# Performance work log

Measured on AMD Instinct MI355X. Metric: run time of the kernel, lower is better.

Reference implementation:

```python
import jax, jax.numpy as jnp
import numpy as np

B, N_MELS, T = 8, 96, 1024
FLUX = 1
N_DIMS = N_MELS * (1 + FLUX)          # 192
C = 32                                 # num_channels
D_MODEL = C * (N_DIMS // 4)            # 1536
N_LAYERS = 4
D_STATE = 16
D_CONV = 4
D_INNER = 2 * D_MODEL                  # 3072 (expand=2)
DT_RANK = -(-D_MODEL // 16)            # 96
N_CLASSES = 5


def setup_inputs() -> dict:
    key = jax.random.key(0)
    ks = iter(jax.random.split(key, 64))
    def rn(shape, scale=0.02):
        return jax.random.normal(next(ks), shape, dtype=jnp.float32) * scale
    p = {}
    p['x'] = jax.random.normal(next(ks), (B, N_MELS, T), dtype=jnp.float32)
    # ResidualBlock 1: conv3x3 -> act -> conv3x3, 1x1 shortcut (channel change 1->C)
    p['c1a_w'] = rn((C, 1, 3, 3)); p['c1a_b'] = jnp.zeros((C,), jnp.float32)
    p['c1b_w'] = rn((C, C, 3, 3)); p['c1b_b'] = jnp.zeros((C,), jnp.float32)
    p['c1s_w'] = rn((C, 1, 1, 1)); p['c1s_b'] = jnp.zeros((C,), jnp.float32)
    # ResidualBlock 2: identity shortcut (C->C)
    p['c2a_w'] = rn((C, C, 3, 3)); p['c2a_b'] = jnp.zeros((C,), jnp.float32)
    p['c2b_w'] = rn((C, C, 3, 3)); p['c2b_b'] = jnp.zeros((C,), jnp.float32)
    # Mamba layers (stacked over layer dim L)
    L = N_LAYERS
    p['norm_w'] = jnp.ones((L, D_MODEL), jnp.float32)
    p['in_w'] = rn((L, 2 * D_INNER, D_MODEL))
    p['conv_w'] = rn((L, D_INNER, D_CONV))
    p['conv_b'] = jnp.zeros((L, D_INNER), jnp.float32)
    p['xproj_w'] = rn((L, DT_RANK + 2 * D_STATE, D_INNER))
    p['dt_w'] = rn((L, D_INNER, DT_RANK))
    p['dt_b'] = rn((L, D_INNER), 0.01)
    A = jnp.tile(jnp.arange(1, D_STATE + 1, dtype=jnp.float32)[None], (D_INNER, 1))
    p['A_log'] = jnp.tile(jnp.log(A)[None], (L, 1, 1))
    p['Dp'] = jnp.ones((L, D_INNER), jnp.float32)
    p['out_w'] = rn((L, D_MODEL, D_INNER))
    p['fc_w'] = rn((N_CLASSES, D_MODEL)); p['fc_b'] = jnp.zeros((N_CLASSES,), jnp.float32)
    return p


def conv2d_same(x, w, b):
    y = jax.lax.conv_general_dilated(x, w, (1, 1), 'SAME',
                                     dimension_numbers=('NCHW', 'OIHW', 'NCHW'))
    return y + b[None, :, None, None]


def res_block(x, wa, ba, wb, bb, ws=None, bs=None):
    h = jax.nn.silu(conv2d_same(x, wa, ba))
    h = conv2d_same(h, wb, bb)
    sc = x if ws is None else conv2d_same(x, ws, bs)
    return jax.nn.silu(h + sc)


def maxpool_f2(x):
    # MaxPool2d(kernel=(2,1), stride=(2,1)) over (freq, time)
    return jax.lax.reduce_window(x, -jnp.inf, jax.lax.max,
                                 (1, 1, 2, 1), (1, 1, 2, 1), 'VALID')


def rmsnorm(x, w, eps=1e-5):
    return x * jax.lax.rsqrt(jnp.mean(x * x, -1, keepdims=True) + eps) * w


def mamba_layer(x, norm_w, in_w, conv_w, conv_b, xproj_w, dt_w, dt_b, A_log, Dp, out_w):
    # x: (B, T, D_MODEL)
    xn = rmsnorm(x, norm_w)
    xz = jnp.einsum('btd,ed->bte', xn, in_w)           # (B,T,2*d_inner)
    u, z = jnp.split(xz, 2, axis=-1)
    # depthwise causal conv over time
    u_t = jnp.transpose(u, (0, 2, 1))                   # (B, d_inner, T)
    u_t = jax.lax.conv_general_dilated(u_t, conv_w[:, None, :], (1,), [(D_CONV - 1, 0)],
                                       dimension_numbers=('NCH', 'OIH', 'NCH'),
                                       feature_group_count=D_INNER)
    u = jax.nn.silu(jnp.transpose(u_t, (0, 2, 1)) + conv_b)
    x_dbl = jnp.einsum('btd,ed->bte', u, xproj_w)
    dt, Bm, Cm = jnp.split(x_dbl, [DT_RANK, DT_RANK + D_STATE], axis=-1)
    delta = jax.nn.softplus(jnp.einsum('btr,dr->btd', dt, dt_w) + dt_b)  # (B,T,d_inner)
    A = -jnp.exp(A_log)                                 # (d_inner, d_state)

    def step(h, inp):
        d_t, u_tt, B_t, C_t = inp                        # (B,di),(B,di),(B,ds),(B,ds)
        dA = jnp.exp(d_t[..., None] * A)                 # (B, d_inner, d_state)
        h = dA * h + (d_t * u_tt)[..., None] * B_t[:, None, :]
        y = jnp.einsum('bds,bs->bd', h, C_t)
        return h, y

    h0 = jnp.zeros((x.shape[0], D_INNER, D_STATE), x.dtype)
    xs = (jnp.moveaxis(delta, 1, 0), jnp.moveaxis(u, 1, 0),
          jnp.moveaxis(Bm, 1, 0), jnp.moveaxis(Cm, 1, 0))
    _, ys = jax.lax.scan(step, h0, xs)
    y = jnp.moveaxis(ys, 0, 1) + u * Dp
    y = y * jax.nn.silu(z)
    return x + jnp.einsum('bte,de->btd', y, out_w)


def reference(x, c1a_w, c1a_b, c1b_w, c1b_b, c1s_w, c1s_b,
              c2a_w, c2a_b, c2b_w, c2b_b,
              norm_w, in_w, conv_w, conv_b, xproj_w, dt_w, dt_b, A_log, Dp, out_w,
              fc_w, fc_b):
    # flux: temporal diff, relu, left-pad on time, stack along freq
    diff = x[..., 1:] - x[..., :-1]
    diff = jax.nn.relu(jnp.pad(diff, ((0, 0), (0, 0), (1, 0))))
    h = jnp.concatenate([x, diff], axis=1)              # (B, n_dims, T)
    h = h[:, None]                                       # (B, 1, n_dims, T)
    h = maxpool_f2(res_block(h, c1a_w, c1a_b, c1b_w, c1b_b, c1s_w, c1s_b))
    h = maxpool_f2(res_block(h, c2a_w, c2a_b, c2b_w, c2b_b))
    h = h.reshape(h.shape[0], -1, h.shape[3])            # (B, C*(n_dims//4), T)
    h = jnp.transpose(h, (0, 2, 1))                      # (B, T, d_model)
    for l in range(N_LAYERS):
        h = mamba_layer(h, norm_w[l], in_w[l], conv_w[l], conv_b[l], xproj_w[l],
                        dt_w[l], dt_b[l], A_log[l], Dp[l], out_w[l])
    logits = jnp.einsum('btd,cd->btc', h, fc_w) + fc_b
    return jax.nn.silu(jnp.transpose(logits, (0, 2, 1)))  # (B, n_classes, T)
```

## Files before the change

### kernel.cpp

```cpp
#include <hip/hip_runtime.h>
#include <cstdint>
#include <cstddef>

#define DEV static __device__ __forceinline__

typedef unsigned short u16;
typedef unsigned int   u32;
typedef __bf16 bf16x8 __attribute__((ext_vector_type(8)));
typedef float  f32x4  __attribute__((ext_vector_type(4)));

namespace {
constexpr int NB     = 8;
constexpr int NT     = 1024;
constexpr int NMEL   = 96;
constexpr int NDIM   = 192;
constexpr int NCH    = 32;
constexpr int DMODEL = 1536;
constexpr int DINNER = 3072;
constexpr int DSTATE = 16;
constexpr int DTRANK = 96;
constexpr int NLAYER = 4;
constexpr int NCLASS = 5;
constexpr int MROWS  = NB * NT;
constexpr int NCHK   = 16;
constexpr int CHKT   = NT / NCHK;
}

DEV float siluf(float x)    { return x / (1.0f + __expf(-x)); }
DEV float softplusf(float x){ return fmaxf(x, 0.0f) + log1pf(__expf(-fabsf(x))); }

DEV u16 f2bf(float f) {
    u32 u = __float_as_uint(f);
    u32 r = u + 0x7FFFu + ((u >> 16) & 1u);
    return (u16)(r >> 16);
}
DEV float bf2f(u16 h) { return __uint_as_float(((u32)h) << 16); }

DEV f32x4 exp2v(f32x4 x) {
    f32x4 r;
    r[0] = exp2f(x[0]); r[1] = exp2f(x[1]);
    r[2] = exp2f(x[2]); r[3] = exp2f(x[3]);
    return r;
}

#define GLD(gp, lp) __builtin_amdgcn_global_load_lds( \
    (const __attribute__((address_space(1))) u32*)(const void*)(gp), \
    (__attribute__((address_space(3))) u32*)(void*)(lp), 16, 0, 0)

__global__ void k_zero(u16* p) { p[threadIdx.x] = 0; }

__global__ __launch_bounds__(256) void k_prep(const float* __restrict__ x,
                                              float* __restrict__ hcat)
{
    int idx = blockIdx.x * 256 + threadIdx.x;
    if (idx >= NB * NDIM * NT) return;
    int t = idx & (NT - 1);
    int m = (idx >> 10) % NDIM;
    int b = idx / (NDIM * NT);
    float v;
    if (m < NMEL) {
        v = x[((size_t)b * NMEL + m) * NT + t];
    } else {
        int mm = m - NMEL;
        v = 0.f;
        if (t > 0) {
            const float* p = x + ((size_t)b * NMEL + mm) * NT + t;
            v = fmaxf(p[0] - p[-1], 0.f);
        }
    }
    hcat[idx] = v;
}

__global__ __launch_bounds__(256) void k_wconv(const float* __restrict__ w,
    u16* __restrict__ dh, u16* __restrict__ dl)
{
    int idx = blockIdx.x * 256 + threadIdx.x;
    if (idx >= 9216) return;
    int ci = idx & 31, cout = (idx >> 5) & 31, tap = idx >> 10;
    float v = w[((size_t)cout * 32 + ci) * 9 + tap];
    u16 h = f2bf(v);
    dh[idx] = h;
    dl[idx] = f2bf(v - bf2f(h));
}

__global__ __launch_bounds__(256) void k_conv1a(const float* __restrict__ hcat,
    const float* __restrict__ w, const float* __restrict__ bias,
    u16* __restrict__ oh, u16* __restrict__ ol)
{
    int idx = blockIdx.x * 256 + threadIdx.x;
    if (idx >= NB * NDIM * NT) return;
    int t = idx & (NT - 1);
    int h = (idx >> 10) % NDIM;
    int b = idx / (NDIM * NT);
    float in[3][3];
    #pragma unroll
    for (int dh = 0; dh < 3; ++dh)
        #pragma unroll
        for (int dw = 0; dw < 3; ++dw) {
            int hh = h + dh - 1, tt = t + dw - 1;
            in[dh][dw] = (hh >= 0 && hh < NDIM && tt >= 0 && tt < NT)
                       ? hcat[((size_t)b * NDIM + hh) * NT + tt] : 0.f;
        }
    u16 hb[32], lb[32];
    #pragma unroll
    for (int c = 0; c < NCH; ++c) {
        float acc = bias[c];
        #pragma unroll
        for (int dh = 0; dh < 3; ++dh)
            #pragma unroll
            for (int dw = 0; dw < 3; ++dw)
                acc = fmaf(in[dh][dw], w[c * 9 + dh * 3 + dw], acc);
        float o = siluf(acc);
        u16 hh2 = f2bf(o);
        hb[c] = hh2;
        lb[c] = f2bf(o - bf2f(hh2));
    }
    size_t ob = (((size_t)b * NDIM + h) * NT + t) * 32;
    #pragma unroll
    for (int j = 0; j < 8; ++j) {
        ushort4 hv = { hb[j*4], hb[j*4+1], hb[j*4+2], hb[j*4+3] };
        ushort4 lv = { lb[j*4], lb[j*4+1], lb[j*4+2], lb[j*4+3] };
        *(ushort4*)(oh + ob + j * 4) = hv;
        *(ushort4*)(ol + ob + j * 4) = lv;
    }
}

template<int VAR>
__global__ __launch_bounds__(256) void k_convmfma(
    const u16* __restrict__ Xh, const u16* __restrict__ Xl,
    const u16* __restrict__ CWh, const u16* __restrict__ CWl,
    const float* __restrict__ hcat, const float* __restrict__ sw, const float* __restrict__ sb,
    const u16* __restrict__ Sh, const u16* __restrict__ Sl,
    const float* __restrict__ bias,
    u16* __restrict__ Oh, u16* __restrict__ Ol,
    float* __restrict__ RES,
    const u16* __restrict__ zeropad)
{
    constexpr int HIN = (VAR == 0) ? 192 : 96;
    __shared__ __align__(16) u16 lds[2][8448];
    const int t0 = blockIdx.x * 64;
    const int ho = blockIdx.y;
    const int b  = blockIdx.z;
    const int tid = threadIdx.x;
    const int wid = tid >> 6, lane = tid & 63;
    const int r0 = 2 * ho - 1;

    for (int cb = wid * 64; cb < 2112; cb += 256) {
        int c = cb + lane;
        int plane = (c >= 1056) ? 1 : 0;
        int cc = c - plane * 1056;
        int row = cc / 264;
        int rc  = cc - row * 264;
        int pos = rc >> 2;
        int slot = rc & 3;
        int cib = slot ^ ((pos >> 1) & 3);
        int h = r0 + row;
        int t = t0 - 1 + pos;
        const u16* bp = plane ? Xl : Xh;
        const u16* src = (h >= 0 && h < HIN && t >= 0 && t < NT)
            ? bp + (((size_t)(b * HIN + h)) * NT + t) * 32 + cib * 8
            : zeropad;
        u16* ldst = &lds[0][0] + (size_t)cb * 8;
        GLD(src, ldst);
    }
    __syncthreads();

    const int fr = lane & 15, fq = lane >> 4;
    f32x4 acc[2][2];
    #pragma unroll
    for (int pr = 0; pr < 2; ++pr)
        #pragma unroll
        for (int mt = 0; mt < 2; ++mt) acc[pr][mt] = (f32x4){0.f, 0.f, 0.f, 0.f};

    #pragma unroll
    for (int dh = 0; dh < 3; ++dh) {
        #pragma unroll
        for (int dt = 0; dt < 3; ++dt) {
            int tap = dh * 3 + dt;
            bf16x8 wh[2], wl[2];
            #pragma unroll
            for (int mt = 0; mt < 2; ++mt) {
                size_t wo = ((size_t)tap * 32 + mt * 16 + fr) * 32 + fq * 8;
                wh[mt] = *(const bf16x8*)(CWh + wo);
                wl[mt] = *(const bf16x8*)(CWl + wo);
            }
            int p = (wid << 4) + fr + dt;
            int sl = fq ^ ((p >> 1) & 3);
            #pragma unroll
            for (int pr = 0; pr < 2; ++pr) {
                int rr = pr + dh;
                const u16* lp = &lds[0][0] + ((rr * 66 + p) * 4 + sl) * 8;
                bf16x8 xh = *(const bf16x8*)lp;
                bf16x8 xl = *(const bf16x8*)(lp + 8448);
                #pragma unroll
                for (int mt = 0; mt < 2; ++mt) {
                    acc[pr][mt] = __builtin_amdgcn_mfma_f32_16x16x32_bf16(wh[mt], xh, acc[pr][mt], 0, 0, 0);
                    acc[pr][mt] = __builtin_amdgcn_mfma_f32_16x16x32_bf16(wh[mt], xl, acc[pr][mt], 0, 0, 0);
                    acc[pr][mt] = __builtin_amdgcn_mfma_f32_16x16x32_bf16(wl[mt], xh, acc[pr][mt], 0, 0, 0);
                }
            }
        }
    }

    const int t = t0 + (wid << 4) + fr;
    float hc0 = 0.f, hc1 = 0.f;
    if (VAR == 0) {
        hc0 = hcat[((size_t)(b * NDIM + 2 * ho    )) * NT + t];
        hc1 = hcat[((size_t)(b * NDIM + 2 * ho + 1)) * NT + t];
    }
    #pragma unroll
    for (int mt = 0; mt < 2; ++mt) {
        float v0[4], v1[4];
        if (VAR == 2) {
            ushort4 s0h = *(const ushort4*)(Sh + (((size_t)(b * 96 + 2 * ho    )) * NT + t) * 32 + mt * 16 + fq * 4);
            ushort4 s0l = *(const ushort4*)(Sl + (((size_t)(b * 96 + 2 * ho    )) * NT + t) * 32 + mt * 16 + fq * 4);
            ushort4 s1h = *(const ushort4*)(Sh + (((size_t)(b * 96 + 2 * ho + 1)) * NT + t) * 32 + mt * 16 + fq * 4);
            ushort4 s1l = *(const ushort4*)(Sl + (((size_t)(b * 96 + 2 * ho + 1)) * NT + t) * 32 + mt * 16 + fq * 4);
            v0[0] = bf2f(s0h.x) + bf2f(s0l.x); v0[1] = bf2f(s0h.y) + bf2f(s0l.y);
            v0[2] = bf2f(s0h.z) + bf2f(s0l.z); v0[3] = bf2f(s0h.w) + bf2f(s0l.w);
            v1[0] = bf2f(s1h.x) + bf2f(s1l.x); v1[1] = bf2f(s1h.y) + bf2f(s1l.y);
            v1[2] = bf2f(s1h.z) + bf2f(s1l.z); v1[3] = bf2f(s1h.w) + bf2f(s1l.w);
        }
        u16 hs[4], ls[4];
        float r0v[4], r1v[4];
        #pragma unroll
        for (int r = 0; r < 4; ++r) {
            int c = mt * 16 + fq * 4 + r;
            float a0 = acc[0][mt][r] + bias[c];
            float a1 = acc[1][mt][r] + bias[c];
            if (VAR == 0) {
                a0 += fmaf(hc0, sw[c], sb[c]);
                a1 += fmaf(hc1, sw[c], sb[c]);
            }
            if (VAR == 2) { a0 += v0[r]; a1 += v1[r]; }
            a0 = siluf(a0); a1 = siluf(a1);
            if (VAR == 1) { r0v[r] = a0; r1v[r] = a1; }
            else {
                float m = fmaxf(a0, a1);
                if (VAR == 2) r0v[r] = m;
                else { u16 hh = f2bf(m); hs[r] = hh; ls[r] = f2bf(m - bf2f(hh)); }
            }
        }
        if (VAR == 0) {
            size_t ob = (((size_t)(b * 96 + ho)) * NT + t) * 32 + mt * 16 + fq * 4;
            ushort4 hv = { hs[0], hs[1], hs[2], hs[3] };
            ushort4 lv = { ls[0], ls[1], ls[2], ls[3] };
            *(ushort4*)(Oh + ob) = hv;
            *(ushort4*)(Ol + ob) = lv;
        } else if (VAR == 1) {
            #pragma unroll
            for (int pr = 0; pr < 2; ++pr) {
                size_t ob = (((size_t)(b * 96 + 2 * ho + pr)) * NT + t) * 32 + mt * 16 + fq * 4;
                u16 hh[4], ll[4];
                #pragma unroll
                for (int r = 0; r < 4; ++r) {
                    float m = pr ? r1v[r] : r0v[r];
                    hh[r] = f2bf(m); ll[r] = f2bf(m - bf2f(hh[r]));
                }
                ushort4 hv = { hh[0], hh[1], hh[2], hh[3] };
                ushort4 lv = { ll[0], ll[1], ll[2], ll[3] };
                *(ushort4*)(Oh + ob) = hv;
                *(ushort4*)(Ol + ob) = lv;
            }
        } else {
            #pragma unroll
            for (int r = 0; r < 4; ++r) {
                int c = mt * 16 + fq * 4 + r;
                RES[((size_t)b * NT + t) * DMODEL + c * 48 + ho] = r0v[r];
            }
        }
    }
}

__global__ __launch_bounds__(256) void k_rmsnorm(const float* __restrict__ in,
    const float* __restrict__ w, u16* __restrict__ oh, u16* __restrict__ ol)
{
    int row = blockIdx.x;
    int tid = threadIdx.x;
    const float* p = in + (size_t)row * DMODEL;
    float v[6]; float ss = 0.f;
    #pragma unroll
    for (int j = 0; j < 6; ++j) { v[j] = p[tid + j * 256]; ss = fmaf(v[j], v[j], ss); }
    #pragma unroll
    for (int off = 1; off < 64; off <<= 1) ss += __shfl_xor(ss, off);
    __shared__ float red[4];
    int lane = tid & 63, wv = tid >> 6;
    if (lane == 0) red[wv] = ss;
    __syncthreads();
    float tot = red[0] + red[1] + red[2] + red[3];
    float sc = rsqrtf(tot * (1.0f / DMODEL) + 1e-5f);
    #pragma unroll
    for (int j = 0; j < 6; ++j) {
        int col = tid + j * 256;
        float xv = v[j] * sc * w[col];
        u16 h = f2bf(xv);
        oh[(size_t)row * DMODEL + col] = h;
        ol[(size_t)row * DMODEL + col] = f2bf(xv - bf2f(h));
    }
}

__global__ __launch_bounds__(256) void k_split(const float* __restrict__ src,
    u16* __restrict__ dh, u16* __restrict__ dl, int n4)
{
    int idx = blockIdx.x * 256 + threadIdx.x;
    if (idx >= n4) return;
    float4 v = ((const float4*)src)[idx];
    u16 h0 = f2bf(v.x), h1 = f2bf(v.y), h2 = f2bf(v.z), h3 = f2bf(v.w);
    u16 l0 = f2bf(v.x - bf2f(h0)), l1 = f2bf(v.y - bf2f(h1));
    u16 l2 = f2bf(v.z - bf2f(h2)), l3 = f2bf(v.w - bf2f(h3));
    uint2 hv = { (u32)h0 | ((u32)h1 << 16), (u32)h2 | ((u32)h3 << 16) };
    uint2 lv = { (u32)l0 | ((u32)l1 << 16), (u32)l2 | ((u32)l3 << 16) };
    ((uint2*)dh)[idx] = hv;
    ((uint2*)dl)[idx] = lv;
}

__global__ __launch_bounds__(256) void k_wsplit_pad(const float* __restrict__ src,
    u16* __restrict__ dh, u16* __restrict__ dl)
{
    int idx = blockIdx.x * 256 + threadIdx.x;
    if (idx >= DINNER * 128) return;
    int col = idx & 127, row = idx >> 7;
    float v = (col < DTRANK) ? src[(size_t)row * DTRANK + col] : 0.f;
    u16 h = f2bf(v);
    dh[idx] = h;
    dl[idx] = f2bf(v - bf2f(h));
}

template<int EPI>
__global__ __launch_bounds__(256, 4) void k_gemm_mfma(
    const u16* __restrict__ Ahi, const u16* __restrict__ Alo, int lda,
    const u16* __restrict__ Bhi, const u16* __restrict__ Blo, int ldb,
    float* __restrict__ C, int ldc, int Ktot,
    const float* __restrict__ bias, size_t zStride)
{
    __shared__ __align__(16) u16 lds[4][4096];
    const int tid = threadIdx.x;
    const int m0 = blockIdx.y * 128, n0 = blockIdx.x * 128;
    const int kPer = Ktot / gridDim.z;
    const int kBase = blockIdx.z * kPer;
    const int wid = tid >> 6, lane = tid & 63;
    const int wr = wid >> 1, wc = wid & 1;
    const int fr = lane & 15, fq = lane >> 4;
    const int srow  = tid >> 2;
    const int sslot = (tid & 3) ^ ((srow >> 1) & 3);

    f32x4 acc[4][4];
    #pragma unroll
    for (int mi = 0; mi < 4; ++mi)
        #pragma unroll
        for (int ni = 0; ni < 4; ++ni) acc[mi][ni] = (f32x4){0.f, 0.f, 0.f, 0.f};

    for (int k0 = kBase; k0 < kBase + kPer; k0 += 32) {
        #pragma unroll
        for (int i = 0; i < 2; ++i) {
            int row = i * 64 + srow;
            size_t offA = (size_t)(m0 + row) * lda + k0 + sslot * 8;
            size_t offB = (size_t)(n0 + row) * ldb + k0 + sslot * 8;
            u16* lb = &lds[0][0] + i * 2048 + (wid << 9);
            GLD(Ahi + offA, lb);
            GLD(Alo + offA, lb + 4096);
            GLD(Bhi + offB, lb + 8192);
            GLD(Blo + offB, lb + 12288);
        }
        __syncthreads();
        bf16x8 ah[4], al[4], bh[4], bl[4];
        #pragma unroll
        for (int mi = 0; mi < 4; ++mi) {
            int row = wr * 64 + mi * 16 + fr;
            int sl  = fq ^ ((row >> 1) & 3);
            const u16* p = &lds[0][row * 32 + sl * 8];
            ah[mi] = *(const bf16x8*)p;
            al[mi] = *(const bf16x8*)(p + 4096);
        }
        #pragma unroll
        for (int ni = 0; ni < 4; ++ni) {
            int row = wc * 64 + ni * 16 + fr;
            int sl  = fq ^ ((row >> 1) & 3);
            const u16* p = &lds[2][row * 32 + sl * 8];
            bh[ni] = *(const bf16x8*)p;
            bl[ni] = *(const bf16x8*)(p + 4096);
        }
        #pragma unroll
        for (int mi = 0; mi < 4; ++mi)
            #pragma unroll
            for (int ni = 0; ni < 4; ++ni) {
                acc[mi][ni] = __builtin_amdgcn_mfma_f32_16x16x32_bf16(ah[mi], bh[ni], acc[mi][ni], 0, 0, 0);
                acc[mi][ni] = __builtin_amdgcn_mfma_f32_16x16x32_bf16(ah[mi], bl[ni], acc[mi][ni], 0, 0, 0);
                acc[mi][ni] = __builtin_amdgcn_mfma_f32_16x16x32_bf16(al[mi], bh[ni], acc[mi][ni], 0, 0, 0);
            }
        __syncthreads();
    }

    float* Cz = C + (EPI == 0 ? (size_t)blockIdx.z * zStride : (size_t)0);
    #pragma unroll
    for (int mi = 0; mi < 4; ++mi)
        #pragma unroll
        for (int ni = 0; ni < 4; ++ni) {
            int gr = m0 + wr * 64 + mi * 16 + fq * 4;
            int gc = n0 + wc * 64 + ni * 16 + fr;
            float* cp = Cz + (size_t)gr * ldc + gc;
            #pragma unroll
            for (int r = 0; r < 4; ++r) {
                float v = acc[mi][ni][r];
                if (EPI == 1) v = softplusf(v + bias[gc]);
                if (EPI == 2) v += cp[(size_t)r * ldc];
                cp[(size_t)r * ldc] = v;
            }
        }
}

__global__ __launch_bounds__(256) void k_conv1d(
    const float* __restrict__ xz, const float* __restrict__ w,
    const float* __restrict__ bias, u16* __restrict__ uh, u16* __restrict__ ul)
{
    constexpr int CT = 16;
    const int d  = (blockIdx.x * 256 + threadIdx.x) * 2;
    const int t0 = blockIdx.y * CT;
    const int b  = blockIdx.z;
    float4 w0 = *(const float4*)(w + (size_t)d * 4);
    float4 w1 = *(const float4*)(w + (size_t)(d + 1) * 4);
    float2 bb = *(const float2*)(bias + d);
    const float* xp = xz + ((size_t)b * NT + t0) * (2 * DINNER) + d;
    float2 a0 = {0.f, 0.f}, a1 = {0.f, 0.f}, a2 = {0.f, 0.f};
    if (t0 > 0) {
        a0 = *(const float2*)(xp - 3 * 2 * DINNER);
        a1 = *(const float2*)(xp - 2 * 2 * DINNER);
        a2 = *(const float2*)(xp - 1 * 2 * DINNER);
    }
    u32* uhp = (u32*)(uh + ((size_t)b * NT + t0) * DINNER + d);
    u32* ulp = (u32*)(ul + ((size_t)b * NT + t0) * DINNER + d);
    #pragma unroll
    for (int t = 0; t < CT; ++t) {
        float2 a3 = *(const float2*)(xp + (size_t)t * 2 * DINNER);
        float o0 = siluf(bb.x + a0.x * w0.x + a1.x * w0.y + a2.x * w0.z + a3.x * w0.w);
        float o1 = siluf(bb.y + a0.y * w1.x + a1.y * w1.y + a2.y * w1.z + a3.y * w1.w);
        u16 h0 = f2bf(o0), h1 = f2bf(o1);
        u16 l0 = f2bf(o0 - bf2f(h0)), l1 = f2bf(o1 - bf2f(h1));
        uhp[(size_t)t * (DINNER / 2)] = (u32)h0 | ((u32)h1 << 16);
        ulp[(size_t)t * (DINNER / 2)] = (u32)l0 | ((u32)l1 << 16);
        a0 = a1; a1 = a2; a2 = a3;
    }
}

__global__ __launch_bounds__(256) void k_reduce_split(const float* __restrict__ part,
    float* __restrict__ out, u16* __restrict__ dh, u16* __restrict__ dl)
{
    int idx = blockIdx.x * 256 + threadIdx.x;
    if (idx >= MROWS * 128) return;
    float s = part[idx] + part[(size_t)1 * MROWS * 128 + idx]
            + part[(size_t)2 * MROWS * 128 + idx] + part[(size_t)3 * MROWS * 128 + idx];
    out[idx] = s;
    u16 h = f2bf(s);
    dh[idx] = h;
    dl[idx] = f2bf(s - bf2f(h));
}

__global__ __launch_bounds__(256) void k_scan_p1(
    const float* __restrict__ xz, const u16* __restrict__ uh, const u16* __restrict__ ul,
    const float* __restrict__ xdbl, const float* __restrict__ A_log,
    float* __restrict__ HP, float* __restrict__ SS)
{
    const int d = blockIdx.x * 256 + threadIdx.x;
    const int c = blockIdx.y, b = blockIdx.z;
    const float L2E = 1.44269504088896340736f;
    f32x4 al0 = *(const f32x4*)(A_log + (size_t)d * DSTATE + 0);
    f32x4 al1 = *(const f32x4*)(A_log + (size_t)d * DSTATE + 4);
    f32x4 al2 = *(const f32x4*)(A_log + (size_t)d * DSTATE + 8);
    f32x4 al3 = *(const f32x4*)(A_log + (size_t)d * DSTATE + 12);
    f32x4 aa0, aa1, aa2, aa3;
    #pragma unroll
    for (int j = 0; j < 4; ++j) {
        aa0[j] = -__expf(al0[j]) * L2E;
        aa1[j] = -__expf(al1[j]) * L2E;
        aa2[j] = -__expf(al2[j]) * L2E;
        aa3[j] = -__expf(al3[j]) * L2E;
    }
    const int t0 = c * CHKT;
    const float* dP = xz + ((size_t)b * NT + t0) * (2 * DINNER) + d;
    const u16* uhP = uh + ((size_t)b * NT + t0) * DINNER + d;
    const u16* ulP = ul + ((size_t)b * NT + t0) * DINNER + d;
    const float* bP = xdbl + ((size_t)b * NT + t0) * 128 + DTRANK;
    f32x4 h0 = {0.f,0.f,0.f,0.f}, h1 = h0, h2 = h0, h3 = h0;
    float S = 0.f;
    float dlt = dP[0];
    float uu = bf2f(uhP[0]) + bf2f(ulP[0]);
    for (int t = 0; t < CHKT; ++t) {
        float dlt_n = 0.f, uu_n = 0.f;
        if (t + 1 < CHKT) {
            dlt_n = dP[2 * DINNER];
            uu_n = bf2f(uhP[DINNER]) + bf2f(ulP[DINNER]);
        }
        f32x4 B0 = *(const f32x4*)(bP + 0);
        f32x4 B1 = *(const f32x4*)(bP + 4);
        f32x4 B2 = *(const f32x4*)(bP + 8);
        f32x4 B3 = *(const f32x4*)(bP + 12);
        float du = dlt * uu;
        S += dlt;
        h0 = exp2v(dlt * aa0) * h0 + du * B0;
        h1 = exp2v(dlt * aa1) * h1 + du * B1;
        h2 = exp2v(dlt * aa2) * h2 + du * B2;
        h3 = exp2v(dlt * aa3) * h3 + du * B3;
        dP += 2 * DINNER; uhP += DINNER; ulP += DINNER; bP += 128;
        dlt = dlt_n; uu = uu_n;
    }
    size_t a = (((size_t)(b * NCHK + c) * DINNER) + d) * DSTATE;
    *(f32x4*)(HP + a + 0)  = h0;
    *(f32x4*)(HP + a + 4)  = h1;
    *(f32x4*)(HP + a + 8)  = h2;
    *(f32x4*)(HP + a + 12) = h3;
    SS[(size_t)(b * NCHK + c) * DINNER + d] = S;
}

__global__ __launch_bounds__(256) void k_scan_p2(float* __restrict__ HP,
    const float* __restrict__ SS, const float* __restrict__ A_log)
{
    int idx = blockIdx.x * 256 + threadIdx.x;
    if (idx >= NB * DINNER * DSTATE) return;
    int s = idx & (DSTATE - 1);
    int d = (idx >> 4) % DINNER;
    int b = idx / (DINNER * DSTATE);
    const float L2E = 1.44269504088896340736f;
    float aa = -__expf(A_log[d * DSTATE + s]) * L2E;
    float h = 0.f;
    #pragma unroll
    for (int c = 0; c < NCHK; ++c) {
        size_t a = (((size_t)(b * NCHK + c) * DINNER) + d) * DSTATE + s;
        float hc = HP[a];
        float P = exp2f(aa * SS[(size_t)(b * NCHK + c) * DINNER + d]);
        HP[a] = h;
        h = fmaf(P, h, hc);
    }
}

__global__ __launch_bounds__(256) void k_scan_p3(
    const float* __restrict__ xz,
    u16* uh, u16* ul,
    const float* __restrict__ xdbl,
    const float* __restrict__ A_log, const float* __restrict__ Dp,
    const float* __restrict__ HP)
{
    const int d = blockIdx.x * 256 + threadIdx.x;
    const int c = blockIdx.y, b = blockIdx.z;
    const float L2E = 1.44269504088896340736f;
    f32x4 al0 = *(const f32x4*)(A_log + (size_t)d * DSTATE + 0);
    f32x4 al1 = *(const f32x4*)(A_log + (size_t)d * DSTATE + 4);
    f32x4 al2 = *(const f32x4*)(A_log + (size_t)d * DSTATE + 8);
    f32x4 al3 = *(const f32x4*)(A_log + (size_t)d * DSTATE + 12);
    f32x4 aa0, aa1, aa2, aa3;
    #pragma unroll
    for (int j = 0; j < 4; ++j) {
        aa0[j] = -__expf(al0[j]) * L2E;
        aa1[j] = -__expf(al1[j]) * L2E;
        aa2[j] = -__expf(al2[j]) * L2E;
        aa3[j] = -__expf(al3[j]) * L2E;
    }
    const float dp = Dp[d];
    const int t0 = c * CHKT;
    const float* dP = xz + ((size_t)b * NT + t0) * (2 * DINNER) + d;
    const float* zP = dP + DINNER;
    const u16* uhP = uh + ((size_t)b * NT + t0) * DINNER + d;
    const u16* ulP = ul + ((size_t)b * NT + t0) * DINNER + d;
    u16* yhP = (u16*)uhP;
    u16* ylP = (u16*)ulP;
    const float* bP = xdbl + ((size_t)b * NT + t0) * 128 + DTRANK;
    size_t ha = (((size_t)(b * NCHK + c) * DINNER) + d) * DSTATE;
    f32x4 h0 = *(const f32x4*)(HP + ha + 0);
    f32x4 h1 = *(const f32x4*)(HP + ha + 4);
    f32x4 h2 = *(const f32x4*)(HP + ha + 8);
    f32x4 h3 = *(const f32x4*)(HP + ha + 12);
    float dlt = dP[0], zz = zP[0];
    float uu = bf2f(uhP[0]) + bf2f(ulP[0]);
    for (int t = 0; t < CHKT; ++t) {
        float dlt_n = 0.f, uu_n = 0.f, zz_n = 0.f;
        if (t + 1 < CHKT) {
            dlt_n = dP[2 * DINNER]; zz_n = zP[2 * DINNER];
            uu_n = bf2f(uhP[DINNER]) + bf2f(ulP[DINNER]);
        }
        f32x4 B0 = *(const f32x4*)(bP + 0);
        f32x4 B1 = *(const f32x4*)(bP + 4);
        f32x4 B2 = *(const f32x4*)(bP + 8);
        f32x4 B3 = *(const f32x4*)(bP + 12);
        f32x4 C0 = *(const f32x4*)(bP + DSTATE + 0);
        f32x4 C1 = *(const f32x4*)(bP + DSTATE + 4);
        f32x4 C2 = *(const f32x4*)(bP + DSTATE + 8);
        f32x4 C3 = *(const f32x4*)(bP + DSTATE + 12);
        float du = dlt * uu;
        h0 = exp2v(dlt * aa0) * h0 + du * B0;
        h1 = exp2v(dlt * aa1) * h1 + du * B1;
        h2 = exp2v(dlt * aa2) * h2 + du * B2;
        h3 = exp2v(dlt * aa3) * h3 + du * B3;
        f32x4 pv = h0 * C0 + h1 * C1 + h2 * C2 + h3 * C3;
        float p = (pv[0] + pv[1]) + (pv[2] + pv[3]);
        float yv = (p + uu * dp) * siluf(zz);
        u16 hh = f2bf(yv);
        yhP[0] = hh;
        ylP[0] = f2bf(yv - bf2f(hh));
        dP += 2 * DINNER; zP += 2 * DINNER;
        uhP += DINNER; ulP += DINNER; yhP += DINNER; ylP += DINNER;
        bP += 128;
        dlt = dlt_n; zz = zz_n; uu = uu_n;
    }
}

__global__ __launch_bounds__(256) void k_fc(const float* __restrict__ hR,
    const float* __restrict__ w, const float* __restrict__ bias,
    float* __restrict__ out)
{
    int row = blockIdx.x;
    int tid = threadIdx.x;
    const float* p = hR + (size_t)row * DMODEL;
    float acc[NCLASS] = {0.f, 0.f, 0.f, 0.f, 0.f};
    #pragma unroll
    for (int j = 0; j < 6; ++j) {
        int col = tid + j * 256;
        float v = p[col];
        #pragma unroll
        for (int c = 0; c < NCLASS; ++c)
            acc[c] = fmaf(v, w[c * DMODEL + col], acc[c]);
    }
    #pragma unroll
    for (int c = 0; c < NCLASS; ++c)
        #pragma unroll
        for (int off = 1; off < 64; off <<= 1)
            acc[c] += __shfl_xor(acc[c], off);
    __shared__ float red[4][NCLASS];
    int lane = tid & 63, wv = tid >> 6;
    if (lane == 0)
        for (int c = 0; c < NCLASS; ++c) red[wv][c] = acc[c];
    __syncthreads();
    if (tid < NCLASS) {
        float s = red[0][tid] + red[1][tid] + red[2][tid] + red[3][tid] + bias[tid];
        int b = row >> 10, t = row & (NT - 1);
        out[((size_t)b * NCLASS + tid) * NT + t] = siluf(s);
    }
}

extern "C" void kernel_launch(void* const* d_in, const int* in_sizes, int n_in,
                              void* d_out, int out_size, void* d_ws, size_t ws_size,
                              hipStream_t stream)
{
    const float* x      = (const float*)d_in[0];
    const float* c1a_w  = (const float*)d_in[1];
    const float* c1a_b  = (const float*)d_in[2];
    const float* c1b_w  = (const float*)d_in[3];
    const float* c1b_b  = (const float*)d_in[4];
    const float* c1s_w  = (const float*)d_in[5];
    const float* c1s_b  = (const float*)d_in[6];
    const float* c2a_w  = (const float*)d_in[7];
    const float* c2a_b  = (const float*)d_in[8];
    const float* c2b_w  = (const float*)d_in[9];
    const float* c2b_b  = (const float*)d_in[10];
    const float* norm_w = (const float*)d_in[11];
    const float* in_w   = (const float*)d_in[12];
    const float* conv_w = (const float*)d_in[13];
    const float* conv_b = (const float*)d_in[14];
    const float* xproj_w= (const float*)d_in[15];
    const float* dt_w   = (const float*)d_in[16];
    const float* dt_b   = (const float*)d_in[17];
    const float* A_log  = (const float*)d_in[18];
    const float* Dp     = (const float*)d_in[19];
    const float* out_w  = (const float*)d_in[20];
    const float* fc_w   = (const float*)d_in[21];
    const float* fc_b   = (const float*)d_in[22];
    float* outp = (float*)d_out;
    (void)in_sizes; (void)n_in; (void)out_size; (void)ws_size;

    char* base = (char*)d_ws;
    size_t off = 0;
    auto takeB = [&](size_t bytes) { void* p = base + off; off = (off + bytes + 255) & ~(size_t)255; return p; };
    float* HCAT = (float*)takeB((size_t)NB * NDIM * NT * 4);
    float* XZ   = (float*)takeB((size_t)MROWS * 2 * DINNER * 4);
    float* RES  = (float*)takeB((size_t)MROWS * DMODEL * 4);
    u16*   XNh  = (u16*)takeB((size_t)MROWS * DMODEL * 2);
    u16*   XNl  = (u16*)takeB((size_t)MROWS * DMODEL * 2);
    u16*   Uh   = (u16*)takeB((size_t)MROWS * DINNER * 2);
    u16*   Ul   = (u16*)takeB((size_t)MROWS * DINNER * 2);
    float* XDBL = (float*)takeB((size_t)MROWS * 128 * 4);
    float* XPART= (float*)takeB((size_t)4 * MROWS * 128 * 4);
    u16*   XDh  = (u16*)takeB((size_t)MROWS * 128 * 2);
    u16*   XDl  = (u16*)takeB((size_t)MROWS * 128 * 2);
    u16*   Wh   = (u16*)takeB((size_t)9437184 * 2);
    u16*   Wl   = (u16*)takeB((size_t)9437184 * 2);
    float* HP   = (float*)takeB((size_t)NB * NCHK * DINNER * DSTATE * 4);
    float* SS   = (float*)takeB((size_t)NB * NCHK * DINNER * 4);
    u16*   CW1h = (u16*)takeB(18432);
    u16*   CW1l = (u16*)takeB(18432);
    u16*   CW2h = (u16*)takeB(18432);
    u16*   CW2l = (u16*)takeB(18432);
    u16*   CW3h = (u16*)takeB(18432);
    u16*   CW3l = (u16*)takeB(18432);
    u16*   ZPAD = (u16*)takeB(256);

    u16* T1h = (u16*)XZ;
    u16* T1l = T1h + (size_t)NB * NDIM * NT * 32;
    u16* T3h = (u16*)XZ;
    u16* T3l = T3h + (size_t)NB * NDIM * NT * 32;
    u16* P1h = Uh;
    u16* P1l = Ul;

    const int n1 = NB * NDIM * NT;
    k_zero<<<1, 128, 0, stream>>>(ZPAD);
    k_prep  <<<(n1 + 255) / 256, 256, 0, stream>>>(x, HCAT);
    k_wconv<<<36, 256, 0, stream>>>(c1b_w, CW1h, CW1l);
    k_wconv<<<36, 256, 0, stream>>>(c2a_w, CW2h, CW2l);
    k_wconv<<<36, 256, 0, stream>>>(c2b_w, CW3h, CW3l);
    k_conv1a<<<(n1 + 255) / 256, 256, 0, stream>>>(HCAT, c1a_w, c1a_b, T1h, T1l);
    k_convmfma<0><<<dim3(16, 96, NB), 256, 0, stream>>>(
        T1h, T1l, CW1h, CW1l, HCAT, c1s_w, c1s_b, nullptr, nullptr,
        c1b_b, P1h, P1l, nullptr, ZPAD);
    k_convmfma<1><<<dim3(16, 48, NB), 256, 0, stream>>>(
        P1h, P1l, CW2h, CW2l, nullptr, nullptr, nullptr, nullptr, nullptr,
        c2a_b, T3h, T3l, nullptr, ZPAD);
    k_convmfma<2><<<dim3(16, 48, NB), 256, 0, stream>>>(
        T3h, T3l, CW3h, CW3l, nullptr, nullptr, nullptr, P1h, P1l,
        c2b_b, nullptr, nullptr, RES, ZPAD);

    for (int l = 0; l < NLAYER; ++l) {
        k_rmsnorm<<<MROWS, 256, 0, stream>>>(RES, norm_w + (size_t)l * DMODEL, XNh, XNl);
        k_split<<<(9437184 / 4 + 255) / 256, 256, 0, stream>>>(
            in_w + (size_t)l * 2 * DINNER * DMODEL, Wh, Wl, 9437184 / 4);
        k_gemm_mfma<0><<<dim3(2 * DINNER / 128, MROWS / 128, 1), 256, 0, stream>>>(
            XNh, XNl, DMODEL, Wh, Wl, DMODEL, XZ, 2 * DINNER, DMODEL, nullptr, 0);
        k_conv1d<<<dim3(DINNER / 512, NT / 16, NB), 256, 0, stream>>>(
            XZ, conv_w + (size_t)l * DINNER * 4, conv_b + (size_t)l * DINNER, Uh, Ul);
        k_split<<<(393216 / 4 + 255) / 256, 256, 0, stream>>>(
            xproj_w + (size_t)l * 128 * DINNER, Wh, Wl, 393216 / 4);
        k_gemm_mfma<0><<<dim3(1, MROWS / 128, 4), 256, 0, stream>>>(
            Uh, Ul, DINNER, Wh, Wl, DINNER, XPART, 128, DINNER, nullptr, (size_t)MROWS * 128);
        k_reduce_split<<<(MROWS * 128 + 255) / 256, 256, 0, stream>>>(XPART, XDBL, XDh, XDl);
        k_wsplit_pad<<<(DINNER * 128 + 255) / 256, 256, 0, stream>>>(
            dt_w + (size_t)l * DINNER * DTRANK, Wh, Wl);
        k_gemm_mfma<1><<<dim3(DINNER / 128, MROWS / 128, 1), 256, 0, stream>>>(
            XDh, XDl, 128, Wh, Wl, 128, XZ, 2 * DINNER, 128,
            dt_b + (size_t)l * DINNER, 0);
        k_scan_p1<<<dim3(DINNER / 256, NCHK, NB), 256, 0, stream>>>(
            XZ, Uh, Ul, XDBL, A_log + (size_t)l * DINNER * DSTATE, HP, SS);
        k_scan_p2<<<(NB * DINNER * DSTATE + 255) / 256, 256, 0, stream>>>(
            HP, SS, A_log + (size_t)l * DINNER * DSTATE);
        k_scan_p3<<<dim3(DINNER / 256, NCHK, NB), 256, 0, stream>>>(
            XZ, Uh, Ul, XDBL, A_log + (size_t)l * DINNER * DSTATE,
            Dp + (size_t)l * DINNER, HP);
        k_split<<<(4718592 / 4 + 255) / 256, 256, 0, stream>>>(
            out_w + (size_t)l * DMODEL * DINNER, Wh, Wl, 4718592 / 4);
        k_gemm_mfma<2><<<dim3(DMODEL / 128, MROWS / 128, 1), 256, 0, stream>>>(
            Uh, Ul, DINNER, Wh, Wl, DINNER, RES, DMODEL, DINNER, nullptr, 0);
    }
    k_fc<<<MROWS, 256, 0, stream>>>(RES, fc_w, fc_b, outp);
}
```

Baseline: 5.341 ms.

## Add double-buffered 256x256 GEMM for in_proj/out_proj; deepen K-tile in 128 GEMM

Adds a new 512-thread GEMM kernel with 256x256 output tiles and double-buffered LDS staging. It prefetches the next K-slice while MFMAs run and raises wave priority around the MFMA blocks. This kernel replaces the 128x128 GEMM for the two large projections (in_proj and out_proj). The remaining 128x128 kernel now uses K=64 per iteration with a wider XOR swizzle and drops its occupancy hint, so its loads and syncs cover more work each. The larger tiles cut global re-reads and barrier overhead, but they add register pressure and lower occupancy, and the out_proj grid shrinks to 6x32 blocks.

```diff
diff --git a/kernel.cpp b/kernel.cpp
--- a/kernel.cpp
+++ b/kernel.cpp
@@ -327,13 +327,13 @@
 }
 
 template<int EPI>
-__global__ __launch_bounds__(256, 4) void k_gemm_mfma(
+__global__ __launch_bounds__(256) void k_gemm_mfma(
     const u16* __restrict__ Ahi, const u16* __restrict__ Alo, int lda,
     const u16* __restrict__ Bhi, const u16* __restrict__ Blo, int ldb,
     float* __restrict__ C, int ldc, int Ktot,
     const float* __restrict__ bias, size_t zStride)
 {
-    __shared__ __align__(16) u16 lds[4][4096];
+    __shared__ __align__(16) u16 lds[4][8192];
     const int tid = threadIdx.x;
     const int m0 = blockIdx.y * 128, n0 = blockIdx.x * 128;
     const int kPer = Ktot / gridDim.z;
@@ -341,8 +341,8 @@
     const int wid = tid >> 6, lane = tid & 63;
     const int wr = wid >> 1, wc = wid & 1;
     const int fr = lane & 15, fq = lane >> 4;
-    const int srow  = tid >> 2;
-    const int sslot = (tid & 3) ^ ((srow >> 1) & 3);
+    const int srow  = tid >> 3;
+    const int sslot = (tid & 7) ^ ((tid >> 3) & 7);
 
     f32x4 acc[4][4];
     #pragma unroll
@@ -350,44 +350,47 @@
         #pragma unroll
         for (int ni = 0; ni < 4; ++ni) acc[mi][ni] = (f32x4){0.f, 0.f, 0.f, 0.f};
 
-    for (int k0 = kBase; k0 < kBase + kPer; k0 += 32) {
-        #pragma unroll
-        for (int i = 0; i < 2; ++i) {
-            int row = i * 64 + srow;
+    for (int k0 = kBase; k0 < kBase + kPer; k0 += 64) {
+        #pragma unroll
+        for (int i = 0; i < 4; ++i) {
+            int row = i * 32 + srow;
             size_t offA = (size_t)(m0 + row) * lda + k0 + sslot * 8;
             size_t offB = (size_t)(n0 + row) * ldb + k0 + sslot * 8;
             u16* lb = &lds[0][0] + i * 2048 + (wid << 9);
             GLD(Ahi + offA, lb);
-            GLD(Alo + offA, lb + 4096);
-            GLD(Bhi + offB, lb + 8192);
-            GLD(Blo + offB, lb + 12288);
+            GLD(Alo + offA, lb + 8192);
+            GLD(Bhi + offB, lb + 16384);
+            GLD(Blo + offB, lb + 24576);
         }
         __syncthreads();
-        bf16x8 ah[4], al[4], bh[4], bl[4];
-        #pragma unroll
-        for (int mi = 0; mi < 4; ++mi) {
-            int row = wr * 64 + mi * 16 + fr;
-            int sl  = fq ^ ((row >> 1) & 3);
-            const u16* p = &lds[0][row * 32 + sl * 8];
-            ah[mi] = *(const bf16x8*)p;
-            al[mi] = *(const bf16x8*)(p + 4096);
-        }
-        #pragma unroll
-        for (int ni = 0; ni < 4; ++ni) {
-            int row = wc * 64 + ni * 16 + fr;
-            int sl  = fq ^ ((row >> 1) & 3);
-            const u16* p = &lds[2][row * 32 + sl * 8];
-            bh[ni] = *(const bf16x8*)p;
-            bl[ni] = *(const bf16x8*)(p + 4096);
-        }
-        #pragma unroll
-        for (int mi = 0; mi < 4; ++mi)
+        #pragma unroll
+        for (int h = 0; h < 2; ++h) {
+            bf16x8 ah[4], al[4], bh[4], bl[4];
+            #pragma unroll
+            for (int mi = 0; mi < 4; ++mi) {
+                int row = wr * 64 + mi * 16 + fr;
+                int sl  = (h * 4 + fq) ^ (row & 7);
+                const u16* p = &lds[0][row * 64 + sl * 8];
+                ah[mi] = *(const bf16x8*)p;
+                al[mi] = *(const bf16x8*)(p + 8192);
+            }
             #pragma unroll
             for (int ni = 0; ni < 4; ++ni) {
-                acc[mi][ni] = __builtin_amdgcn_mfma_f32_16x16x32_bf16(ah[mi], bh[ni], acc[mi][ni], 0, 0, 0);
-                acc[mi][ni] = __builtin_amdgcn_mfma_f32_16x16x32_bf16(ah[mi], bl[ni], acc[mi][ni], 0, 0, 0);
-                acc[mi][ni] = __builtin_amdgcn_mfma_f32_16x16x32_bf16(al[mi], bh[ni], acc[mi][ni], 0, 0, 0);
-            }
+                int row = wc * 64 + ni * 16 + fr;
+                int sl  = (h * 4 + fq) ^ (row & 7);
+                const u16* p = &lds[2][row * 64 + sl * 8];
+                bh[ni] = *(const bf16x8*)p;
+                bl[ni] = *(const bf16x8*)(p + 8192);
+            }
+            #pragma unroll
+            for (int mi = 0; mi < 4; ++mi)
+                #pragma unroll
+                for (int ni = 0; ni < 4; ++ni) {
+                    acc[mi][ni] = __builtin_amdgcn_mfma_f32_16x16x32_bf16(ah[mi], bh[ni], acc[mi][ni], 0, 0, 0);
+                    acc[mi][ni] = __builtin_amdgcn_mfma_f32_16x16x32_bf16(ah[mi], bl[ni], acc[mi][ni], 0, 0, 0);
+                    acc[mi][ni] = __builtin_amdgcn_mfma_f32_16x16x32_bf16(al[mi], bh[ni], acc[mi][ni], 0, 0, 0);
+                }
+        }
         __syncthreads();
     }
 
@@ -403,6 +406,104 @@
             for (int r = 0; r < 4; ++r) {
                 float v = acc[mi][ni][r];
                 if (EPI == 1) v = softplusf(v + bias[gc]);
+                if (EPI == 2) v += cp[(size_t)r * ldc];
+                cp[(size_t)r * ldc] = v;
+            }
+        }
+}
+
+template<int EPI>
+__global__ __launch_bounds__(512, 2) void k_gemm256(
+    const u16* __restrict__ Ahi, const u16* __restrict__ Alo, int lda,
+    const u16* __restrict__ Bhi, const u16* __restrict__ Blo, int ldb,
+    float* __restrict__ C, int ldc, int Ktot)
+{
+    __shared__ __align__(16) u16 lds[2 * 4 * 256 * 32];
+    const int tid = threadIdx.x;
+    const int m0 = blockIdx.y * 256, n0 = blockIdx.x * 256;
+    const int wid = tid >> 6, lane = tid & 63;
+    const int wr = wid >> 2, wc = wid & 3;
+    const int fr = lane & 15, fq = lane >> 4;
+    const int nK = Ktot / 32;
+    const int srow  = tid >> 2;
+    const int sslot = (tid & 3) ^ ((srow >> 1) & 3);
+
+    auto STAGE = [&](int buf, int k0, int h) {
+        int p = h >> 1, hb = h & 1;
+        int row = hb * 128 + srow;
+        const u16* gp;
+        if (p == 0)      gp = Ahi + (size_t)(m0 + row) * lda + k0 + sslot * 8;
+        else if (p == 1) gp = Alo + (size_t)(m0 + row) * lda + k0 + sslot * 8;
+        else if (p == 2) gp = Bhi + (size_t)(n0 + row) * ldb + k0 + sslot * 8;
+        else             gp = Blo + (size_t)(n0 + row) * ldb + k0 + sslot * 8;
+        u16* ldst = lds + ((size_t)((buf * 4 + p) * 256 + hb * 128 + wid * 16) * 32);
+        GLD(gp, ldst);
+    };
+
+    f32x4 acc[8][4];
+    #pragma unroll
+    for (int mi = 0; mi < 8; ++mi)
+        #pragma unroll
+        for (int ni = 0; ni < 4; ++ni) acc[mi][ni] = (f32x4){0.f, 0.f, 0.f, 0.f};
+
+    #pragma unroll
+    for (int h = 0; h < 8; ++h) STAGE(0, 0, h);
+
+    for (int kt = 0; kt < nK; ++kt) {
+        const int cur = kt & 1;
+        __syncthreads();
+        const int k1 = (kt + 1) * 32;
+        const bool pf = (kt + 1 < nK);
+        bf16x8 bh[4], bl[4];
+        #pragma unroll
+        for (int q = 0; q < 4; ++q) {
+            if (q < 2 && pf) {
+                #pragma unroll
+                for (int j = 0; j < 4; ++j) STAGE(cur ^ 1, k1, q * 4 + j);
+            }
+            if (q == 0) {
+                #pragma unroll
+                for (int ni = 0; ni < 4; ++ni) {
+                    int row = wc * 64 + ni * 16 + fr;
+                    int sl  = fq ^ ((row >> 1) & 3);
+                    const u16* p = lds + ((size_t)((cur * 4 + 2) * 256 + row) * 32) + sl * 8;
+                    bh[ni] = *(const bf16x8*)p;
+                    bl[ni] = *(const bf16x8*)(p + 256 * 32);
+                }
+            }
+            bf16x8 ah[2], al[2];
+            #pragma unroll
+            for (int j = 0; j < 2; ++j) {
+                int row = wr * 128 + (2 * q + j) * 16 + fr;
+                int sl  = fq ^ ((row >> 1) & 3);
+                const u16* p = lds + ((size_t)((cur * 4 + 0) * 256 + row) * 32) + sl * 8;
+                ah[j] = *(const bf16x8*)p;
+                al[j] = *(const bf16x8*)(p + 256 * 32);
+            }
+            __builtin_amdgcn_s_barrier();
+            __builtin_amdgcn_s_setprio(1);
+            #pragma unroll
+            for (int j = 0; j < 2; ++j)
+                #pragma unroll
+                for (int ni = 0; ni < 4; ++ni) {
+                    acc[2 * q + j][ni] = __builtin_amdgcn_mfma_f32_16x16x32_bf16(ah[j], bh[ni], acc[2 * q + j][ni], 0, 0, 0);
+                    acc[2 * q + j][ni] = __builtin_amdgcn_mfma_f32_16x16x32_bf16(ah[j], bl[ni], acc[2 * q + j][ni], 0, 0, 0);
+                    acc[2 * q + j][ni] = __builtin_amdgcn_mfma_f32_16x16x32_bf16(al[j], bh[ni], acc[2 * q + j][ni], 0, 0, 0);
+                }
+            __builtin_amdgcn_s_setprio(0);
+        }
+    }
+
+    #pragma unroll
+    for (int mi = 0; mi < 8; ++mi)
+        #pragma unroll
+        for (int ni = 0; ni < 4; ++ni) {
+            int gr = m0 + wr * 128 + mi * 16 + fq * 4;
+            int gc = n0 + wc * 64 + ni * 16 + fr;
+            float* cp = C + (size_t)gr * ldc + gc;
+            #pragma unroll
+            for (int r = 0; r < 4; ++r) {
+                float v = acc[mi][ni][r];
                 if (EPI == 2) v += cp[(size_t)r * ldc];
                 cp[(size_t)r * ldc] = v;
             }
@@ -719,8 +820,8 @@
         k_rmsnorm<<<MROWS, 256, 0, stream>>>(RES, norm_w + (size_t)l * DMODEL, XNh, XNl);
         k_split<<<(9437184 / 4 + 255) / 256, 256, 0, stream>>>(
             in_w + (size_t)l * 2 * DINNER * DMODEL, Wh, Wl, 9437184 / 4);
-        k_gemm_mfma<0><<<dim3(2 * DINNER / 128, MROWS / 128, 1), 256, 0, stream>>>(
-            XNh, XNl, DMODEL, Wh, Wl, DMODEL, XZ, 2 * DINNER, DMODEL, nullptr, 0);
+        k_gemm256<0><<<dim3(2 * DINNER / 256, MROWS / 256), 512, 0, stream>>>(
+            XNh, XNl, DMODEL, Wh, Wl, DMODEL, XZ, 2 * DINNER, DMODEL);
         k_conv1d<<<dim3(DINNER / 512, NT / 16, NB), 256, 0, stream>>>(
             XZ, conv_w + (size_t)l * DINNER * 4, conv_b + (size_t)l * DINNER, Uh, Ul);
         k_split<<<(393216 / 4 + 255) / 256, 256, 0, stream>>>(
@@ -742,8 +843,8 @@
             Dp + (size_t)l * DINNER, HP);
         k_split<<<(4718592 / 4 + 255) / 256, 256, 0, stream>>>(
             out_w + (size_t)l * DMODEL * DINNER, Wh, Wl, 4718592 / 4);
-        k_gemm_mfma<2><<<dim3(DMODEL / 128, MROWS / 128, 1), 256, 0, stream>>>(
-            Uh, Ul, DINNER, Wh, Wl, DINNER, RES, DMODEL, DINNER, nullptr, 0);
+        k_gemm256<2><<<dim3(DMODEL / 256, MROWS / 256), 512, 0, stream>>>(
+            Uh, Ul, DINNER, Wh, Wl, DINNER, RES, DMODEL, DINNER);
     }
     k_fc<<<MROWS, 256, 0, stream>>>(RES, fc_w, fc_b, outp);
 }
```

After: 4.848 ms. -9.2%, faster.
